# Performance work log

Measured on AMD Instinct MI355X. Metric: run time of the kernel, lower is better.

The kernel has to match this reference:

```python
import jax, jax.numpy as jnp
import numpy as np

N_LOC, N_EVT, E = 100000, 200000, 1000000
F_LOC, F_EVT, H = 128, 128, 64


def setup_inputs() -> dict:
    key = jax.random.key(0)
    ks = jax.random.split(key, 12)
    s = lambda k, shp: jax.random.normal(k, shp, dtype=jnp.float32) * (1.0 / np.sqrt(shp[0]))
    return {
        "loc_x": jax.random.normal(ks[0], (N_LOC, F_LOC), dtype=jnp.float32),
        "evt_x": jax.random.normal(ks[1], (N_EVT, F_EVT), dtype=jnp.float32),
        "edge_index": jax.random.randint(ks[2], (2, E), 0, N_LOC, dtype=jnp.int64),
        # projections (stored as (in, out))
        "W_loc": s(ks[3], (F_LOC, H)), "b_loc": jnp.zeros((H,), jnp.float32),
        "W_evt": s(ks[4], (F_EVT, H)), "b_evt": jnp.zeros((H,), jnp.float32),
        # SAGEConv: lin_l (on aggregated src, with bias), lin_r (on dst root, no bias)
        "W_l": s(ks[5], (H, H)), "b_l": jnp.zeros((H,), jnp.float32),
        "W_r": s(ks[6], (H, H)),
        # head MLP
        "W_h1": s(ks[7], (H, H // 2)), "b_h1": jnp.zeros((H // 2,), jnp.float32),
        "W_h2": s(ks[8], (H // 2, 1)), "b_h2": jnp.zeros((1,), jnp.float32),
    }


def reference(loc_x, evt_x, edge_index, W_loc, b_loc, W_evt, b_evt,
              W_l, b_l, W_r, W_h1, b_h1, W_h2, b_h2):
    # node projections + ReLU
    loc_h = jax.nn.relu(loc_x @ W_loc + b_loc)   # [N_loc, H]
    evt_h = jax.nn.relu(evt_x @ W_evt + b_evt)   # [N_evt, H]

    src, dst = edge_index[0], edge_index[1]      # event -> location
    n_loc = loc_h.shape[0]
    # mean aggregation of source (event) features onto destination (location) nodes
    msg_sum = jax.ops.segment_sum(evt_h[src], dst, num_segments=n_loc)   # [N_loc, H]
    cnt = jax.ops.segment_sum(jnp.ones_like(dst, dtype=loc_h.dtype), dst,
                              num_segments=n_loc)
    agg = msg_sum / jnp.maximum(cnt, 1.0)[:, None]
    # SAGEConv: lin_l(agg) + lin_r(root), then ReLU
    loc_h = jax.nn.relu(agg @ W_l + b_l + loc_h @ W_r)

    # prediction head
    h = jax.nn.relu(loc_h @ W_h1 + b_h1)
    logits = (h @ W_h2 + b_h2)[:, 0]             # [N_loc]
    return logits
```

## Files before the change

### kernel.cpp

```cpp
#include <hip/hip_runtime.h>


#define N_LOC 100000
#define N_EVT 200000
#define E_CNT 1000000
#define NTILES 6250
#define NBKT   256
#define BKT_L  391
#define CAPG   6000
#define QCAP   32
#define BKT_BLK 512
#define PERB   1954

#define PROJ_EVT_BLK 512
#define PROJ_LOC_BLK 256
#define PROJ_BLK_TOT (PROJ_EVT_BLK + PROJ_LOC_BLK)
#define EVT_TILES 12500
#define LOC_TILES 6250
#define HEAD_BLK  512

typedef __attribute__((ext_vector_type(8))) short short8;
typedef __attribute__((ext_vector_type(4))) float floatx4;

__device__ __forceinline__ float b2f(unsigned short u) {
    unsigned int x = ((unsigned int)u) << 16;
    return __builtin_bit_cast(float, x);
}
__device__ __forceinline__ unsigned short f2b(float f) {
    unsigned int x = __builtin_bit_cast(unsigned int, f);
    unsigned int r = (x + 0x7fffu + ((x >> 16) & 1u)) >> 16;
    return (unsigned short)r;
}
__device__ __forceinline__ float loadf(const void* p, int f32, size_t i) {
    return f32 ? ((const float*)p)[i] : b2f(((const unsigned short*)p)[i]);
}

__global__ __launch_bounds__(256) void prep_kernel(
    const void* t0, const void* t1, const int* eidx,
    const void* t3, const void* t4, const void* t5, const void* t6,
    const void* t7, const void* t8, const void* t9, const void* t10,
    const void* t11, const void* t12, const void* t13,
    int* flags, int* gbc, unsigned short* __restrict__ wp_all) {
    int b = blockIdx.x, tid = threadIdx.x;
    __shared__ int s0, s1;

    if (b == 14) { gbc[tid] = 0; return; }

    if (b >= 15) {
        int pb = b - 15;
        const void* W; int K, N, bstart, off;
        if (pb < 4)       { W = t5;  K = 128; N = 64; bstart = 0;  off = 0; }
        else if (pb < 8)  { W = t3;  K = 128; N = 64; bstart = 4;  off = 8192; }
        else if (pb < 10) { W = t7;  K = 64;  N = 64; bstart = 8;  off = 16384; }
        else if (pb < 12) { W = t9;  K = 64;  N = 64; bstart = 10; off = 20480; }
        else              { W = t10; K = 64;  N = 32; bstart = 12; off = 24576; }
        if (tid == 0) s0 = 0;
        __syncthreads();
        int nsamp = 2 * K * N; if (nsamp > 1024) nsamp = 1024;
        const unsigned short* h = (const unsigned short*)W;
        int susp = 0;
        for (int i = tid; i < nsamp; i += 256)
            if (((h[i] >> 7) & 0xFF) >= 0x90) susp++;
        if (susp) atomicAdd(&s0, susp);
        __syncthreads();
        int f32 = (s0 * 16 >= nsamp) ? 1 : 0;

        int idx  = (pb - bstart) * 256 + tid;
        int nk   = K >> 5;
        int f    = idx >> 6;
        int lane = idx & 63;
        int t  = f / nk;
        int kk = f - t * nk;
        int n  = t * 16 + (lane & 15);
        int k0 = kk * 32 + (lane >> 4) * 8;
        unsigned short tmp[8];
#pragma unroll
        for (int j = 0; j < 8; ++j) {
            size_t src = (size_t)(k0 + j) * N + n;
            tmp[j] = f32 ? f2b(((const float*)W)[src])
                         : ((const unsigned short*)W)[src];
        }
#pragma unroll
        for (int j = 0; j < 8; ++j) wp_all[(size_t)off + (size_t)idx * 8 + j] = tmp[j];
        return;
    }

    if (tid == 0) { s0 = 0; s1 = 0; }
    __syncthreads();
    if (b == 13) {
        if (tid < 128) {
            if (eidx[2 * tid] != 0) atomicAdd(&s0, 1);
            if (eidx[2 * tid + 1] != 0) atomicAdd(&s1, 1);
        }
        __syncthreads();
        if (tid == 0) flags[2] = (s1 == 0 && s0 > 32) ? 1 : 0;
        return;
    }
    const void* ptrs[13] = {t0, t1, t3, t4, t5, t6, t7, t8, t9, t10, t11, t12, t13};
    const int   cnts[13] = {12800000, 25600000, 8192, 64, 8192, 64,
                            4096, 64, 4096, 2048, 32, 32, 1};
    const int   slot[13] = {0, 1, 3, 4, 5, 6, 7, 8, 9, 10, 11, 12, 13};
    int nsamp = 2 * cnts[b];
    if (nsamp > 1024) nsamp = 1024;
    const unsigned short* h = (const unsigned short*)ptrs[b];
    int susp = 0;
    for (int i = tid; i < nsamp; i += 256)
        if (((h[i] >> 7) & 0xFF) >= 0x90) susp++;
    if (susp) atomicAdd(&s0, susp);
    __syncthreads();
    if (tid == 0) flags[slot[b]] = (s0 * 16 >= nsamp) ? 1 : 0;
}

__global__ __launch_bounds__(256, 3) void proj_both_kernel(
    const void* __restrict__ evt_x, const void* __restrict__ loc_x,
    const unsigned short* __restrict__ wp_all,
    const void* __restrict__ b_evt, const void* __restrict__ b_loc,
    unsigned short* __restrict__ evt_h, unsigned short* __restrict__ loc_h,
    const int* __restrict__ flags) {
    __shared__ unsigned short bs[8192];
    int blk = blockIdx.x;
    int tid = threadIdx.x, lane = tid & 63, wv = tid >> 6;
    int l15 = lane & 15, quad = lane >> 4;

    const void* X; const unsigned short* Wp; const void* bias;
    unsigned short* Y; int fx, fb, w0, nw, ntile;
    if (blk < PROJ_EVT_BLK) {
        X = evt_x; Wp = wp_all;        bias = b_evt; Y = evt_h;
        fx = flags[1]; fb = flags[6];
        w0 = blk * 4 + wv; nw = PROJ_EVT_BLK * 4; ntile = EVT_TILES;
    } else {
        X = loc_x; Wp = wp_all + 8192; bias = b_loc; Y = loc_h;
        fx = flags[0]; fb = flags[4];
        w0 = (blk - PROJ_EVT_BLK) * 4 + wv; nw = PROJ_LOC_BLK * 4; ntile = LOC_TILES;
    }

    {
        const short8* src = reinterpret_cast<const short8*>(Wp);
        short8* dst = reinterpret_cast<short8*>(bs);
#pragma unroll
        for (int i = 0; i < 4; ++i) dst[tid + i * 256] = src[tid + i * 256];
    }
    __syncthreads();

    float bv[4];
#pragma unroll
    for (int q = 0; q < 4; ++q) bv[q] = loadf(bias, fb, q * 16 + l15);

    if (w0 >= ntile) return;

    auto mfma_store = [&](const short8* a, int t) {
        floatx4 acc[4];
#pragma unroll
        for (int q = 0; q < 4; ++q) acc[q] = (floatx4)0.0f;
#pragma unroll
        for (int q = 0; q < 4; ++q) {
            short8 bq[4];
#pragma unroll
            for (int kk = 0; kk < 4; ++kk)
                bq[kk] = *reinterpret_cast<const short8*>(
                    &bs[((q * 4 + kk) * 64 + lane) * 8]);
#pragma unroll
            for (int kk = 0; kk < 4; ++kk)
                acc[q] = __builtin_amdgcn_mfma_f32_16x16x32_bf16(
                    a[kk], bq[kk], acc[q], 0, 0, 0);
        }
#pragma unroll
        for (int q = 0; q < 4; ++q)
#pragma unroll
            for (int r = 0; r < 4; ++r) {
                float v = acc[q][r] + bv[q];
                v = v > 0.0f ? v : 0.0f;
                Y[(size_t)(t * 16 + quad * 4 + r) * 64 + q * 16 + l15] = f2b(v);
            }
    };

    if (fx) {
        const float* Xf = (const float*)X;
        float4 pf[8];
        auto issueF = [&](int t) {
            const float* xr = Xf + (size_t)(t * 16 + l15) * 128 + quad * 8;
#pragma unroll
            for (int kk = 0; kk < 4; ++kk) {
                pf[kk * 2]     = *reinterpret_cast<const float4*>(xr + kk * 32);
                pf[kk * 2 + 1] = *reinterpret_cast<const float4*>(xr + kk * 32 + 4);
            }
        };
        issueF(w0);
        for (int t = w0; t < ntile; t += nw) {
            short8 a[4];
#pragma unroll
            for (int kk = 0; kk < 4; ++kk) {
                float4 p0 = pf[kk * 2], p1 = pf[kk * 2 + 1];
                short8 v;
                v[0] = (short)f2b(p0.x); v[1] = (short)f2b(p0.y);
                v[2] = (short)f2b(p0.z); v[3] = (short)f2b(p0.w);
                v[4] = (short)f2b(p1.x); v[5] = (short)f2b(p1.y);
                v[6] = (short)f2b(p1.z); v[7] = (short)f2b(p1.w);
                a[kk] = v;
            }
            int tn = t + nw;
            if (tn < ntile) issueF(tn);
            mfma_store(a, t);
        }
    } else {
        const unsigned short* Xh = (const unsigned short*)X;
        short8 an[4];
        auto issueH = [&](int t) {
            const unsigned short* xr = Xh + (size_t)(t * 16 + l15) * 128 + quad * 8;
#pragma unroll
            for (int kk = 0; kk < 4; ++kk)
                an[kk] = *reinterpret_cast<const short8*>(xr + kk * 32);
        };
        issueH(w0);
        for (int t = w0; t < ntile; t += nw) {
            short8 a[4];
#pragma unroll
            for (int kk = 0; kk < 4; ++kk) a[kk] = an[kk];
            int tn = t + nw;
            if (tn < ntile) issueH(tn);
            mfma_store(a, t);
        }
    }
}

__global__ __launch_bounds__(256) void bucket_kernel(
    const int* __restrict__ eidx, uint2* __restrict__ bkt,
    int* __restrict__ gbc, const int* __restrict__ flags) {
    __shared__ uint2 queue[NBKT][QCAP];
    __shared__ int qcnt[NBKT];
    int tid = threadIdx.x, blk = blockIdx.x;
    qcnt[tid] = 0;
    __syncthreads();
    int f64 = flags[2];
    const long long* e64 = (const long long*)eidx;
    int e0 = blk * PERB;
    int e1 = e0 + PERB; if (e1 > E_CNT) e1 = E_CNT;
    const int rounds = (PERB + 255) / 256;

    for (int r = 0; r < rounds; ++r) {
        int e = e0 + r * 256 + tid;
        if (e < e1) {
            int src, dst;
            if (f64) { src = (int)e64[e]; dst = (int)e64[E_CNT + e]; }
            else     { src = eidx[e];     dst = eidx[E_CNT + e]; }
            if ((unsigned)dst < (unsigned)N_LOC && (unsigned)src < (unsigned)N_EVT) {
                int bk = dst / BKT_L;
                int pos = atomicAdd(&qcnt[bk], 1);
                if (pos < QCAP) {
                    queue[bk][pos] = make_uint2((unsigned)src, (unsigned)dst);
                } else {
                    int p = atomicAdd(&gbc[bk], 1);
                    if (p < CAPG) bkt[(size_t)bk * CAPG + p] = make_uint2(src, dst);
                }
            }
        }
        __syncthreads();
        int n = qcnt[tid]; if (n > QCAP) n = QCAP;
        while (n >= 16) {
            int gp = atomicAdd(&gbc[tid], 16);
            if (gp + 16 <= CAPG) {
                uint2* d = bkt + (size_t)tid * CAPG + gp;
#pragma unroll
                for (int j = 0; j < 16; ++j) d[j] = queue[tid][j];
            }
#pragma unroll
            for (int j = 16; j < QCAP; ++j) queue[tid][j - 16] = queue[tid][j];
            n -= 16;
        }
        qcnt[tid] = n;
        __syncthreads();
    }
    int n = qcnt[tid]; if (n > QCAP) n = QCAP;
    if (n > 0) {
        int gp = atomicAdd(&gbc[tid], n);
        for (int j = 0; j < n; ++j)
            if (gp + j < CAPG) bkt[(size_t)tid * CAPG + gp + j] = queue[tid][j];
    }
}

__global__ void scan_gbc_kernel(const int* __restrict__ gbc,
                                int* __restrict__ bbase) {
    __shared__ int sh[256];
    int t = threadIdx.x;
    int v = gbc[t]; if (v > CAPG) v = CAPG;
    sh[t] = v;
    __syncthreads();
    for (int d = 1; d < 256; d <<= 1) {
        int x = (t >= d) ? sh[t - d] : 0;
        __syncthreads();
        sh[t] += x;
        __syncthreads();
    }
    bbase[t] = sh[t] - v;
}

__global__ __launch_bounds__(256) void csr_build_kernel(
    const uint2* __restrict__ bkt, const int* __restrict__ gbc,
    const int* __restrict__ bbase,
    int* __restrict__ rowptr, int* __restrict__ csr) {
    __shared__ int lcnt[512];
    __shared__ int lscan[512];
    __shared__ int lcsr[CAPG];
    int b = blockIdx.x, tid = threadIdx.x;
    int loc0 = b * BKT_L;
    int nloc = N_LOC - loc0; if (nloc > BKT_L) nloc = BKT_L;
    int cntE = gbc[b]; if (cntE > CAPG) cntE = CAPG;
    int base = bbase[b];
    const uint2* bp = bkt + (size_t)b * CAPG;

    int i0 = tid, i1 = tid + 256;
    lcnt[i0] = 0; lcnt[i1] = 0;
    __syncthreads();
    for (int i = tid; i < cntE; i += 256) {
        int d = (int)bp[i].y - loc0;
        atomicAdd(&lcnt[d], 1);
    }
    __syncthreads();
    lscan[i0] = lcnt[i0]; lscan[i1] = lcnt[i1];
    __syncthreads();
    for (int d = 1; d < 512; d <<= 1) {
        int v0 = (i0 >= d) ? lscan[i0 - d] : 0;
        int v1 = (i1 >= d) ? lscan[i1 - d] : 0;
        __syncthreads();
        lscan[i0] += v0; lscan[i1] += v1;
        __syncthreads();
    }
    for (int i = tid; i < nloc; i += 256) {
        int excl = lscan[i] - lcnt[i];
        rowptr[loc0 + i] = base + excl;
        lcnt[i] = excl;
    }
    if (b == NBKT - 1 && tid == 0) rowptr[N_LOC] = base + cntE;
    __syncthreads();
    for (int i = tid; i < cntE; i += 256) {
        uint2 pr = bp[i];
        int d = (int)pr.y - loc0;
        int p = atomicAdd(&lcnt[d], 1);
        if (p < CAPG) lcsr[p] = (int)pr.x;
    }
    __syncthreads();
    for (int i = tid; i < cntE; i += 256) csr[base + i] = lcsr[i];
}

__global__ __launch_bounds__(256) void aggregate_kernel(
    const unsigned short* __restrict__ evt_h,
    const int* __restrict__ rowptr, const int* __restrict__ csr,
    unsigned short* __restrict__ agg, int N) {
    int wid  = (blockIdx.x * 256 + threadIdx.x) >> 6;
    int lane = threadIdx.x & 63;
    if (wid >= N) return;
    int e0 = rowptr[wid], e1 = rowptr[wid + 1];
    float acc = 0.0f;
    for (int j = e0; j < e1; j += 4) {
        int c1 = j + 1 < e1, c2 = j + 2 < e1, c3 = j + 3 < e1;
        int s0 = csr[j];
        int s1 = csr[c1 ? j + 1 : j];
        int s2 = csr[c2 ? j + 2 : j];
        int s3 = csr[c3 ? j + 3 : j];
        float v0 = b2f(evt_h[(size_t)s0 * 64 + lane]);
        float v1 = b2f(evt_h[(size_t)s1 * 64 + lane]);
        float v2 = b2f(evt_h[(size_t)s2 * 64 + lane]);
        float v3 = b2f(evt_h[(size_t)s3 * 64 + lane]);
        acc += v0;
        if (c1) acc += v1;
        if (c2) acc += v2;
        if (c3) acc += v3;
    }
    float inv = (e1 > e0) ? 1.0f / (float)(e1 - e0) : 0.0f;
    agg[(size_t)wid * 64 + lane] = f2b(acc * inv);
}

__global__ __launch_bounds__(256, 3) void head_kernel(
    const unsigned short* __restrict__ agg,
    const unsigned short* __restrict__ loc_h,
    const unsigned short* __restrict__ wp_all,
    const void* __restrict__ bl, const void* __restrict__ bh1,
    const void* __restrict__ wh2, const void* __restrict__ bh2,
    void* __restrict__ out, const int* __restrict__ flags) {
    __shared__ unsigned short bls[4096];
    __shared__ unsigned short brs[4096];
    __shared__ unsigned short b1s[2048];
    __shared__ unsigned short h2s[4][16 * 64];
    int tid = threadIdx.x, lane = tid & 63, wv = tid >> 6;
    int l15 = lane & 15, quad = lane >> 4;
    int fbl = flags[8], fbh1 = flags[11], fwh2 = flags[12], fbh2 = flags[13];
    int fout = flags[0];
    const unsigned short* wp_l  = wp_all + 16384;
    const unsigned short* wp_r  = wp_all + 20480;
    const unsigned short* wp_h1 = wp_all + 24576;

    {
        const short8* sl = reinterpret_cast<const short8*>(wp_l);
        const short8* sr = reinterpret_cast<const short8*>(wp_r);
        const short8* s1 = reinterpret_cast<const short8*>(wp_h1);
        short8* dl = reinterpret_cast<short8*>(bls);
        short8* dr = reinterpret_cast<short8*>(brs);
        short8* d1 = reinterpret_cast<short8*>(b1s);
        dl[tid] = sl[tid]; dl[tid + 256] = sl[tid + 256];
        dr[tid] = sr[tid]; dr[tid + 256] = sr[tid + 256];
        d1[tid] = s1[tid];
    }
    __syncthreads();

    float bbl[4], bh1v[2], w2v[2];
#pragma unroll
    for (int q = 0; q < 4; ++q) bbl[q] = loadf(bl, fbl, q * 16 + l15);
#pragma unroll
    for (int q = 0; q < 2; ++q) {
        bh1v[q] = loadf(bh1, fbh1, q * 16 + l15);
        w2v[q]  = loadf(wh2, fwh2, q * 16 + l15);
    }
    float bb2 = loadf(bh2, fbh2, 0);

    const int NW = HEAD_BLK * 4;
    int w0 = blockIdx.x * 4 + wv;
    if (w0 >= NTILES) return;

    short8 c0[4], c1[4];

    auto issue = [&](short8* c, int t) {
        int m = t * 16 + l15;
#pragma unroll
        for (int kk = 0; kk < 2; ++kk) {
            c[kk]     = *reinterpret_cast<const short8*>(
                agg + (size_t)m * 64 + kk * 32 + quad * 8);
            c[2 + kk] = *reinterpret_cast<const short8*>(
                loc_h + (size_t)m * 64 + kk * 32 + quad * 8);
        }
    };

    auto compute = [&](const short8* c, int tile) {
        floatx4 acc[4];
#pragma unroll
        for (int q = 0; q < 4; ++q) acc[q] = (floatx4)0.0f;
#pragma unroll
        for (int q = 0; q < 4; ++q) {
            short8 bwl[2], bwr[2];
#pragma unroll
            for (int kk = 0; kk < 2; ++kk) {
                bwl[kk] = *reinterpret_cast<const short8*>(
                    &bls[((q * 2 + kk) * 64 + lane) * 8]);
                bwr[kk] = *reinterpret_cast<const short8*>(
                    &brs[((q * 2 + kk) * 64 + lane) * 8]);
            }
#pragma unroll
            for (int kk = 0; kk < 2; ++kk) {
                acc[q] = __builtin_amdgcn_mfma_f32_16x16x32_bf16(
                    c[kk], bwl[kk], acc[q], 0, 0, 0);
                acc[q] = __builtin_amdgcn_mfma_f32_16x16x32_bf16(
                    c[2 + kk], bwr[kk], acc[q], 0, 0, 0);
            }
        }
#pragma unroll
        for (int q = 0; q < 4; ++q)
#pragma unroll
            for (int r = 0; r < 4; ++r) {
                float v = acc[q][r] + bbl[q];
                v = v > 0.0f ? v : 0.0f;
                h2s[wv][(quad * 4 + r) * 64 + q * 16 + l15] = f2b(v);
            }
        short8 aH[2];
#pragma unroll
        for (int kk = 0; kk < 2; ++kk)
            aH[kk] = *reinterpret_cast<const short8*>(
                &h2s[wv][l15 * 64 + kk * 32 + quad * 8]);

        floatx4 a1[2];
#pragma unroll
        for (int q = 0; q < 2; ++q) a1[q] = (floatx4)0.0f;
#pragma unroll
        for (int q = 0; q < 2; ++q) {
            short8 bw1[2];
#pragma unroll
            for (int kk = 0; kk < 2; ++kk)
                bw1[kk] = *reinterpret_cast<const short8*>(
                    &b1s[((q * 2 + kk) * 64 + lane) * 8]);
#pragma unroll
            for (int kk = 0; kk < 2; ++kk)
                a1[q] = __builtin_amdgcn_mfma_f32_16x16x32_bf16(
                    aH[kk], bw1[kk], a1[q], 0, 0, 0);
        }

        float s[4] = {0.f, 0.f, 0.f, 0.f};
#pragma unroll
        for (int q = 0; q < 2; ++q)
#pragma unroll
            for (int r = 0; r < 4; ++r) {
                float v = a1[q][r] + bh1v[q];
                v = v > 0.0f ? v : 0.0f;
                s[r] += v * w2v[q];
            }
#pragma unroll
        for (int r = 0; r < 4; ++r) {
            s[r] += __shfl_xor(s[r], 1);
            s[r] += __shfl_xor(s[r], 2);
            s[r] += __shfl_xor(s[r], 4);
            s[r] += __shfl_xor(s[r], 8);
        }
#pragma unroll
        for (int r = 0; r < 4; ++r) {
            if (l15 == r) {
                int row = tile * 16 + quad * 4 + r;
                float v = s[r] + bb2;
                if (fout) ((float*)out)[row] = v;
                else      ((unsigned short*)out)[row] = f2b(v);
            }
        }
    };

    issue(c0, w0);
    int t = w0;
    while (true) {
        int tn = t + NW;
        bool hn = tn < NTILES;
        if (hn) issue(c1, tn);
        compute(c0, t);
        if (!hn) break;
        t = tn; tn = t + NW; hn = tn < NTILES;
        if (hn) issue(c0, tn);
        compute(c1, t);
        if (!hn) break;
        t = tn;
    }
}

extern "C" void kernel_launch(void* const* d_in, const int* in_sizes, int n_in,
                              void* d_out, int out_size, void* d_ws, size_t ws_size,
                              hipStream_t stream) {
    (void)in_sizes; (void)n_in; (void)out_size; (void)ws_size;
    const void* loc_x = d_in[0];
    const void* evt_x = d_in[1];
    const int*  eidx  = (const int*)d_in[2];
    const void* W_loc = d_in[3];
    const void* b_loc = d_in[4];
    const void* W_evt = d_in[5];
    const void* b_evt = d_in[6];
    const void* W_l   = d_in[7];
    const void* b_l   = d_in[8];
    const void* W_r   = d_in[9];
    const void* W_h1  = d_in[10];
    const void* b_h1  = d_in[11];
    const void* W_h2  = d_in[12];
    const void* b_h2  = d_in[13];

    char* ws = (char*)d_ws;
    unsigned short* evt_h  = (unsigned short*)(ws);
    unsigned short* loc_h  = (unsigned short*)(ws + 25600000);
    int*            csr    = (int*)(ws + 38400000);
    int*            rowptr = (int*)(ws + 42400000);
    int*            gbc    = (int*)(ws + 42800016);
    int*            bbase  = (int*)(ws + 42801040);
    unsigned short* wp_all = (unsigned short*)(ws + 42802064);
    int*            flags  = (int*)(ws + 42855312);
    uint2*          bkt    = (uint2*)(ws + 42855376);
    unsigned short* agg    = (unsigned short*)(ws + 42855376);

    prep_kernel<<<28, 256, 0, stream>>>(
        loc_x, evt_x, eidx, W_loc, b_loc, W_evt, b_evt,
        W_l, b_l, W_r, W_h1, b_h1, W_h2, b_h2,
        flags, gbc, wp_all);

    proj_both_kernel<<<PROJ_BLK_TOT, 256, 0, stream>>>(
        evt_x, loc_x, wp_all, b_evt, b_loc, evt_h, loc_h, flags);

    bucket_kernel<<<BKT_BLK, 256, 0, stream>>>(eidx, bkt, gbc, flags);
    scan_gbc_kernel<<<1, 256, 0, stream>>>(gbc, bbase);
    csr_build_kernel<<<NBKT, 256, 0, stream>>>(bkt, gbc, bbase, rowptr, csr);

    aggregate_kernel<<<(N_LOC + 3) / 4, 256, 0, stream>>>(evt_h, rowptr, csr,
                                                          agg, N_LOC);

    head_kernel<<<HEAD_BLK, 256, 0, stream>>>(
        agg, loc_h, wp_all, b_l, b_h1, W_h2, b_h2, d_out, flags);
}
```

Before: 317.5 us.

## Coalesce projection loads/stores via swizzled LDS staging and vectorize aggregate gathers

The projection kernel now loads each 16-row input tile with fully contiguous per-lane vector loads, stages it in a per-wave XOR-swizzled LDS buffer to rebuild the MFMA operand layout, and stages the output tile through LDS so it can be written with 16-byte coalesced stores instead of scattered 2-byte stores. The aggregate kernel splits a wave into four 16-lane groups, each gathering a different edge's row with 8-byte vector loads, then combines partial sums with cross-lane shuffles. The aim is fewer memory transactions and better coalescing, at the cost of extra LDS traffic and a larger per-block shared memory footprint that could reduce occupancy.

```diff
diff --git a/kernel.cpp b/kernel.cpp
--- a/kernel.cpp
+++ b/kernel.cpp
@@ -21,6 +21,7 @@
 
 typedef __attribute__((ext_vector_type(8))) short short8;
 typedef __attribute__((ext_vector_type(4))) float floatx4;
+typedef __attribute__((ext_vector_type(4))) unsigned short ushort4v;
 
 __device__ __forceinline__ float b2f(unsigned short u) {
     unsigned int x = ((unsigned int)u) << 16;
@@ -118,6 +119,7 @@
     unsigned short* __restrict__ evt_h, unsigned short* __restrict__ loc_h,
     const int* __restrict__ flags) {
     __shared__ unsigned short bs[8192];
+    __shared__ unsigned short at[4][2048];
     int blk = blockIdx.x;
     int tid = threadIdx.x, lane = tid & 63, wv = tid >> 6;
     int l15 = lane & 15, quad = lane >> 4;
@@ -148,7 +150,16 @@
 
     if (w0 >= ntile) return;
 
-    auto mfma_store = [&](const short8* a, int t) {
+    char* myt = (char*)at[wv];
+
+    auto mfma_store = [&](int t) {
+        short8 a[4];
+#pragma unroll
+        for (int kk = 0; kk < 4; ++kk) {
+            int bo = l15 * 256 + kk * 64 + quad * 16;
+            bo ^= (l15 & 7) << 4;
+            a[kk] = *reinterpret_cast<const short8*>(myt + bo);
+        }
         floatx4 acc[4];
 #pragma unroll
         for (int q = 0; q < 4; ++q) acc[q] = (floatx4)0.0f;
@@ -170,55 +181,71 @@
             for (int r = 0; r < 4; ++r) {
                 float v = acc[q][r] + bv[q];
                 v = v > 0.0f ? v : 0.0f;
-                Y[(size_t)(t * 16 + quad * 4 + r) * 64 + q * 16 + l15] = f2b(v);
-            }
+                int row = quad * 4 + r;
+                int bo = row * 128 + (q * 16 + l15) * 2;
+                bo ^= (row & 7) << 4;
+                *reinterpret_cast<unsigned short*>(myt + bo) = f2b(v);
+            }
+#pragma unroll
+        for (int i = 0; i < 2; ++i) {
+            int lin = i * 1024 + lane * 16;
+            int bo = lin ^ (((lane >> 3) & 7) << 4);
+            short8 vv = *reinterpret_cast<const short8*>(myt + bo);
+            *reinterpret_cast<short8*>((char*)Y + (size_t)t * 2048 + lin) = vv;
+        }
     };
 
     if (fx) {
         const float* Xf = (const float*)X;
         float4 pf[8];
         auto issueF = [&](int t) {
-            const float* xr = Xf + (size_t)(t * 16 + l15) * 128 + quad * 8;
-#pragma unroll
-            for (int kk = 0; kk < 4; ++kk) {
-                pf[kk * 2]     = *reinterpret_cast<const float4*>(xr + kk * 32);
-                pf[kk * 2 + 1] = *reinterpret_cast<const float4*>(xr + kk * 32 + 4);
+            const float* xr = Xf + (size_t)t * 2048;
+#pragma unroll
+            for (int i = 0; i < 4; ++i) {
+                pf[i * 2]     = *reinterpret_cast<const float4*>(xr + i * 512 + lane * 8);
+                pf[i * 2 + 1] = *reinterpret_cast<const float4*>(xr + i * 512 + lane * 8 + 4);
             }
         };
         issueF(w0);
         for (int t = w0; t < ntile; t += nw) {
-            short8 a[4];
-#pragma unroll
-            for (int kk = 0; kk < 4; ++kk) {
-                float4 p0 = pf[kk * 2], p1 = pf[kk * 2 + 1];
+#pragma unroll
+            for (int i = 0; i < 4; ++i) {
+                float4 p0 = pf[i * 2], p1 = pf[i * 2 + 1];
                 short8 v;
                 v[0] = (short)f2b(p0.x); v[1] = (short)f2b(p0.y);
                 v[2] = (short)f2b(p0.z); v[3] = (short)f2b(p0.w);
                 v[4] = (short)f2b(p1.x); v[5] = (short)f2b(p1.y);
                 v[6] = (short)f2b(p1.z); v[7] = (short)f2b(p1.w);
-                a[kk] = v;
+                int row = i * 4 + (lane >> 4);
+                int bo = row * 256 + (lane & 15) * 16;
+                bo ^= (row & 7) << 4;
+                *reinterpret_cast<short8*>(myt + bo) = v;
             }
             int tn = t + nw;
             if (tn < ntile) issueF(tn);
-            mfma_store(a, t);
+            mfma_store(t);
         }
     } else {
         const unsigned short* Xh = (const unsigned short*)X;
         short8 an[4];
         auto issueH = [&](int t) {
-            const unsigned short* xr = Xh + (size_t)(t * 16 + l15) * 128 + quad * 8;
-#pragma unroll
-            for (int kk = 0; kk < 4; ++kk)
-                an[kk] = *reinterpret_cast<const short8*>(xr + kk * 32);
+            const unsigned short* xr = Xh + (size_t)t * 2048;
+#pragma unroll
+            for (int i = 0; i < 4; ++i)
+                an[i] = *reinterpret_cast<const short8*>(xr + i * 512 + lane * 8);
         };
         issueH(w0);
         for (int t = w0; t < ntile; t += nw) {
-            short8 a[4];
-#pragma unroll
-            for (int kk = 0; kk < 4; ++kk) a[kk] = an[kk];
+#pragma unroll
+            for (int i = 0; i < 4; ++i) {
+                int row = i * 4 + (lane >> 4);
+                int bo = row * 256 + (lane & 15) * 16;
+                bo ^= (row & 7) << 4;
+                *reinterpret_cast<short8*>(myt + bo) = an[i];
+            }
             int tn = t + nw;
             if (tn < ntile) issueH(tn);
-            mfma_store(a, t);
+            mfma_store(t);
         }
     }
 }
@@ -348,26 +375,32 @@
     unsigned short* __restrict__ agg, int N) {
     int wid  = (blockIdx.x * 256 + threadIdx.x) >> 6;
     int lane = threadIdx.x & 63;
+    int l15 = lane & 15, quad = lane >> 4;
     if (wid >= N) return;
     int e0 = rowptr[wid], e1 = rowptr[wid + 1];
-    float acc = 0.0f;
+    float a0 = 0.f, a1 = 0.f, a2 = 0.f, a3 = 0.f;
     for (int j = e0; j < e1; j += 4) {
-        int c1 = j + 1 < e1, c2 = j + 2 < e1, c3 = j + 3 < e1;
-        int s0 = csr[j];
-        int s1 = csr[c1 ? j + 1 : j];
-        int s2 = csr[c2 ? j + 2 : j];
-        int s3 = csr[c3 ? j + 3 : j];
-        float v0 = b2f(evt_h[(size_t)s0 * 64 + lane]);
-        float v1 = b2f(evt_h[(size_t)s1 * 64 + lane]);
-        float v2 = b2f(evt_h[(size_t)s2 * 64 + lane]);
-        float v3 = b2f(evt_h[(size_t)s3 * 64 + lane]);
-        acc += v0;
-        if (c1) acc += v1;
-        if (c2) acc += v2;
-        if (c3) acc += v3;
-    }
+        int jj = j + quad;
+        bool c = jj < e1;
+        int s = csr[c ? jj : j];
+        ushort4v v = *reinterpret_cast<const ushort4v*>(
+            evt_h + (size_t)s * 64 + l15 * 4);
+        if (c) {
+            a0 += b2f(v[0]); a1 += b2f(v[1]);
+            a2 += b2f(v[2]); a3 += b2f(v[3]);
+        }
+    }
+    a0 += __shfl_xor(a0, 16); a0 += __shfl_xor(a0, 32);
+    a1 += __shfl_xor(a1, 16); a1 += __shfl_xor(a1, 32);
+    a2 += __shfl_xor(a2, 16); a2 += __shfl_xor(a2, 32);
+    a3 += __shfl_xor(a3, 16); a3 += __shfl_xor(a3, 32);
     float inv = (e1 > e0) ? 1.0f / (float)(e1 - e0) : 0.0f;
-    agg[(size_t)wid * 64 + lane] = f2b(acc * inv);
+    if (quad == 0) {
+        ushort4v o;
+        o[0] = f2b(a0 * inv); o[1] = f2b(a1 * inv);
+        o[2] = f2b(a2 * inv); o[3] = f2b(a3 * inv);
+        *reinterpret_cast<ushort4v*>(agg + (size_t)wid * 64 + l15 * 4) = o;
+    }
 }
 
 __global__ __launch_bounds__(256, 3) void head_kernel(
```

Result: no change. 318.6 us (+0.4%).

## Use contiguous per-wave tile ranges, deeper prefetch, and vectorized aggregation gathers

Applied to the files above, without the earlier changes.

The projection and head kernels now give each wave a contiguous range of tiles instead of a grid stride, with an XCD-aware block swizzle so neighbouring ranges share a die. The projection loop double-buffers its prefetch two tiles ahead. The aggregation kernel has each quarter-wave gather a different neighbor row with 8-byte loads and then reduces across quads with shuffles, cutting the number of load instructions per edge. The aim is better DRAM locality and more memory-level parallelism, at the cost of more registers and extra shuffle work.

```diff
diff --git a/kernel.cpp b/kernel.cpp
--- a/kernel.cpp
+++ b/kernel.cpp
@@ -21,6 +21,7 @@
 
 typedef __attribute__((ext_vector_type(8))) short short8;
 typedef __attribute__((ext_vector_type(4))) float floatx4;
+typedef __attribute__((ext_vector_type(4))) unsigned short ushort4v;
 
 __device__ __forceinline__ float b2f(unsigned short u) {
     unsigned int x = ((unsigned int)u) << 16;
@@ -123,15 +124,18 @@
     int l15 = lane & 15, quad = lane >> 4;
 
     const void* X; const unsigned short* Wp; const void* bias;
-    unsigned short* Y; int fx, fb, w0, nw, ntile;
+    unsigned short* Y; int fx, fb, W, nwav, ntile;
     if (blk < PROJ_EVT_BLK) {
+        int sw = (blk & 7) * (PROJ_EVT_BLK / 8) + (blk >> 3);
         X = evt_x; Wp = wp_all;        bias = b_evt; Y = evt_h;
         fx = flags[1]; fb = flags[6];
-        w0 = blk * 4 + wv; nw = PROJ_EVT_BLK * 4; ntile = EVT_TILES;
+        W = sw * 4 + wv; nwav = PROJ_EVT_BLK * 4; ntile = EVT_TILES;
     } else {
+        int b2 = blk - PROJ_EVT_BLK;
+        int sw = (b2 & 7) * (PROJ_LOC_BLK / 8) + (b2 >> 3);
         X = loc_x; Wp = wp_all + 8192; bias = b_loc; Y = loc_h;
         fx = flags[0]; fb = flags[4];
-        w0 = (blk - PROJ_EVT_BLK) * 4 + wv; nw = PROJ_LOC_BLK * 4; ntile = LOC_TILES;
+        W = sw * 4 + wv; nwav = PROJ_LOC_BLK * 4; ntile = LOC_TILES;
     }
 
     {
@@ -146,7 +150,9 @@
 #pragma unroll
     for (int q = 0; q < 4; ++q) bv[q] = loadf(bias, fb, q * 16 + l15);
 
-    if (w0 >= ntile) return;
+    int s = (int)(((long long)W * ntile) / nwav);
+    int e = (int)(((long long)(W + 1) * ntile) / nwav);
+    if (s >= e) return;
 
     auto mfma_store = [&](const short8* a, int t) {
         floatx4 acc[4];
@@ -176,8 +182,8 @@
 
     if (fx) {
         const float* Xf = (const float*)X;
-        float4 pf[8];
-        auto issueF = [&](int t) {
+        float4 p0[8], p1[8];
+        auto issueF = [&](float4* pf, int t) {
             const float* xr = Xf + (size_t)(t * 16 + l15) * 128 + quad * 8;
 #pragma unroll
             for (int kk = 0; kk < 4; ++kk) {
@@ -185,40 +191,56 @@
                 pf[kk * 2 + 1] = *reinterpret_cast<const float4*>(xr + kk * 32 + 4);
             }
         };
-        issueF(w0);
-        for (int t = w0; t < ntile; t += nw) {
+        auto convF = [&](short8* a, const float4* pf) {
+#pragma unroll
+            for (int kk = 0; kk < 4; ++kk) {
+                float4 q0 = pf[kk * 2], q1 = pf[kk * 2 + 1];
+                short8 v;
+                v[0] = (short)f2b(q0.x); v[1] = (short)f2b(q0.y);
+                v[2] = (short)f2b(q0.z); v[3] = (short)f2b(q0.w);
+                v[4] = (short)f2b(q1.x); v[5] = (short)f2b(q1.y);
+                v[6] = (short)f2b(q1.z); v[7] = (short)f2b(q1.w);
+                a[kk] = v;
+            }
+        };
+        issueF(p0, s);
+        if (s + 1 < e) issueF(p1, s + 1);
+        int t = s;
+        while (t < e) {
             short8 a[4];
-#pragma unroll
-            for (int kk = 0; kk < 4; ++kk) {
-                float4 p0 = pf[kk * 2], p1 = pf[kk * 2 + 1];
-                short8 v;
-                v[0] = (short)f2b(p0.x); v[1] = (short)f2b(p0.y);
-                v[2] = (short)f2b(p0.z); v[3] = (short)f2b(p0.w);
-                v[4] = (short)f2b(p1.x); v[5] = (short)f2b(p1.y);
-                v[6] = (short)f2b(p1.z); v[7] = (short)f2b(p1.w);
-                a[kk] = v;
-            }
-            int tn = t + nw;
-            if (tn < ntile) issueF(tn);
+            convF(a, p0);
+            if (t + 2 < e) issueF(p0, t + 2);
             mfma_store(a, t);
+            if (t + 1 >= e) break;
+            convF(a, p1);
+            if (t + 3 < e) issueF(p1, t + 3);
+            mfma_store(a, t + 1);
+            t += 2;
         }
     } else {
         const unsigned short* Xh = (const unsigned short*)X;
-        short8 an[4];
-        auto issueH = [&](int t) {
+        short8 n0[4], n1[4];
+        auto issueH = [&](short8* an, int t) {
             const unsigned short* xr = Xh + (size_t)(t * 16 + l15) * 128 + quad * 8;
 #pragma unroll
             for (int kk = 0; kk < 4; ++kk)
                 an[kk] = *reinterpret_cast<const short8*>(xr + kk * 32);
         };
-        issueH(w0);
-        for (int t = w0; t < ntile; t += nw) {
+        issueH(n0, s);
+        if (s + 1 < e) issueH(n1, s + 1);
+        int t = s;
+        while (t < e) {
             short8 a[4];
 #pragma unroll
-            for (int kk = 0; kk < 4; ++kk) a[kk] = an[kk];
-            int tn = t + nw;
-            if (tn < ntile) issueH(tn);
+            for (int kk = 0; kk < 4; ++kk) a[kk] = n0[kk];
+            if (t + 2 < e) issueH(n0, t + 2);
             mfma_store(a, t);
+            if (t + 1 >= e) break;
+#pragma unroll
+            for (int kk = 0; kk < 4; ++kk) a[kk] = n1[kk];
+            if (t + 3 < e) issueH(n1, t + 3);
+            mfma_store(a, t + 1);
+            t += 2;
         }
     }
 }
@@ -348,26 +370,32 @@
     unsigned short* __restrict__ agg, int N) {
     int wid  = (blockIdx.x * 256 + threadIdx.x) >> 6;
     int lane = threadIdx.x & 63;
+    int l15 = lane & 15, quad = lane >> 4;
     if (wid >= N) return;
     int e0 = rowptr[wid], e1 = rowptr[wid + 1];
-    float acc = 0.0f;
+    float a0 = 0.f, a1 = 0.f, a2 = 0.f, a3 = 0.f;
     for (int j = e0; j < e1; j += 4) {
-        int c1 = j + 1 < e1, c2 = j + 2 < e1, c3 = j + 3 < e1;
-        int s0 = csr[j];
-        int s1 = csr[c1 ? j + 1 : j];
-        int s2 = csr[c2 ? j + 2 : j];
-        int s3 = csr[c3 ? j + 3 : j];
-        float v0 = b2f(evt_h[(size_t)s0 * 64 + lane]);
-        float v1 = b2f(evt_h[(size_t)s1 * 64 + lane]);
-        float v2 = b2f(evt_h[(size_t)s2 * 64 + lane]);
-        float v3 = b2f(evt_h[(size_t)s3 * 64 + lane]);
-        acc += v0;
-        if (c1) acc += v1;
-        if (c2) acc += v2;
-        if (c3) acc += v3;
-    }
+        int jj = j + quad;
+        bool c = jj < e1;
+        int s = csr[c ? jj : j];
+        ushort4v v = *reinterpret_cast<const ushort4v*>(
+            evt_h + (size_t)s * 64 + l15 * 4);
+        if (c) {
+            a0 += b2f(v[0]); a1 += b2f(v[1]);
+            a2 += b2f(v[2]); a3 += b2f(v[3]);
+        }
+    }
+    a0 += __shfl_xor(a0, 16); a0 += __shfl_xor(a0, 32);
+    a1 += __shfl_xor(a1, 16); a1 += __shfl_xor(a1, 32);
+    a2 += __shfl_xor(a2, 16); a2 += __shfl_xor(a2, 32);
+    a3 += __shfl_xor(a3, 16); a3 += __shfl_xor(a3, 32);
     float inv = (e1 > e0) ? 1.0f / (float)(e1 - e0) : 0.0f;
-    agg[(size_t)wid * 64 + lane] = f2b(acc * inv);
+    if (quad == 0) {
+        ushort4v o;
+        o[0] = f2b(a0 * inv); o[1] = f2b(a1 * inv);
+        o[2] = f2b(a2 * inv); o[3] = f2b(a3 * inv);
+        *reinterpret_cast<ushort4v*>(agg + (size_t)wid * 64 + l15 * 4) = o;
+    }
 }
 
 __global__ __launch_bounds__(256, 3) void head_kernel(
@@ -412,9 +440,13 @@
     }
     float bb2 = loadf(bh2, fbh2, 0);
 
+    int blk = blockIdx.x;
+    int sw = (blk & 7) * (HEAD_BLK / 8) + (blk >> 3);
+    int W = sw * 4 + wv;
     const int NW = HEAD_BLK * 4;
-    int w0 = blockIdx.x * 4 + wv;
-    if (w0 >= NTILES) return;
+    int s = (int)(((long long)W * NTILES) / NW);
+    int e = (int)(((long long)(W + 1) * NTILES) / NW);
+    if (s >= e) return;
 
     short8 c0[4], c1[4];
 
@@ -481,42 +513,42 @@
                     aH[kk], bw1[kk], a1[q], 0, 0, 0);
         }
 
-        float s[4] = {0.f, 0.f, 0.f, 0.f};
+        float s4[4] = {0.f, 0.f, 0.f, 0.f};
 #pragma unroll
         for (int q = 0; q < 2; ++q)
 #pragma unroll
             for (int r = 0; r < 4; ++r) {
                 float v = a1[q][r] + bh1v[q];
                 v = v > 0.0f ? v : 0.0f;
-                s[r] += v * w2v[q];
+                s4[r] += v * w2v[q];
             }
 #pragma unroll
         for (int r = 0; r < 4; ++r) {
-            s[r] += __shfl_xor(s[r], 1);
-            s[r] += __shfl_xor(s[r], 2);
-            s[r] += __shfl_xor(s[r], 4);
-            s[r] += __shfl_xor(s[r], 8);
+            s4[r] += __shfl_xor(s4[r], 1);
+            s4[r] += __shfl_xor(s4[r], 2);
+            s4[r] += __shfl_xor(s4[r], 4);
+            s4[r] += __shfl_xor(s4[r], 8);
         }
 #pragma unroll
         for (int r = 0; r < 4; ++r) {
             if (l15 == r) {
                 int row = tile * 16 + quad * 4 + r;
-                float v = s[r] + bb2;
+                float v = s4[r] + bb2;
                 if (fout) ((float*)out)[row] = v;
                 else      ((unsigned short*)out)[row] = f2b(v);
             }
         }
     };
 
-    issue(c0, w0);
-    int t = w0;
+    issue(c0, s);
+    int t = s;
     while (true) {
-        int tn = t + NW;
-        bool hn = tn < NTILES;
+        int tn = t + 1;
+        bool hn = tn < e;
         if (hn) issue(c1, tn);
         compute(c0, t);
         if (!hn) break;
-        t = tn; tn = t + NW; hn = tn < NTILES;
+        t = tn; tn = t + 1; hn = tn < e;
         if (hn) issue(c0, tn);
         compute(c1, t);
         if (!hn) break;
```

New measurement: 330.3 us. 4.0% more time.
